# Optimization experiments

Measured on AMD Instinct MI355X. Metric: run time of the kernel, lower is better.

Reference implementation:

```python
import jax, jax.numpy as jnp
import numpy as np

N_NODES = 100000


def gcn_conv(x, W, b, src, dst, n):
    # PyG GCNConv: add self-loops, symmetric degree normalization,
    # linear transform then scatter-add aggregation at target nodes.
    h = x @ W  # [N, out]
    loop = jnp.arange(n, dtype=src.dtype)
    src_sl = jnp.concatenate([src, loop])
    dst_sl = jnp.concatenate([dst, loop])
    deg = jnp.zeros((n,), dtype=h.dtype).at[dst_sl].add(1.0)  # in-degree incl. self-loop
    dinv = jax.lax.rsqrt(deg)  # deg >= 1 thanks to self-loops
    norm = dinv[src_sl] * dinv[dst_sl]  # [E + N]
    msg = h[src_sl] * norm[:, None]  # gather + scale
    out = jax.ops.segment_sum(msg, dst_sl, num_segments=n)  # scatter-add
    return out + b


def setup_inputs() -> dict:
    key = jax.random.key(0)
    k1, k2, k3, k4 = jax.random.split(key, 4)
    n, e = N_NODES, 3200000
    in_c, hid = 3, 32
    x = jax.random.normal(k1, (n, in_c), dtype=jnp.float32)
    edge_index = jax.random.randint(k2, (2, e), 0, n, dtype=jnp.int64)
    W1 = jax.random.normal(k3, (in_c, hid), dtype=jnp.float32) / np.sqrt(in_c)
    b1 = jnp.zeros((hid,), dtype=jnp.float32)
    W2 = jax.random.normal(k4, (hid, in_c), dtype=jnp.float32) / np.sqrt(hid)
    b2 = jnp.zeros((in_c,), dtype=jnp.float32)
    return {"x": x, "edge_index": edge_index, "W1": W1, "b1": b1, "W2": W2, "b2": b2}


def reference(x, edge_index, W1, b1, W2, b2):
    n = x.shape[0]
    src, dst = edge_index[0], edge_index[1]
    h = jax.nn.relu(gcn_conv(x, W1, b1, src, dst, n))
    dx = gcn_conv(h, W2, b2, src, dst, n)
    return dx
```

## Files before the change

kernel.cpp:

```cpp
#include <hip/hip_runtime.h>

static constexpr int NN = 100000;
static constexpr int NE = 3200000;

static constexpr int BKT_D = 200;
static constexpr int NBUCK = NN / BKT_D;
static constexpr unsigned BMUL = 167773u;
static constexpr int BSH = 25;
static constexpr int CAP = 7296;

__device__ __forceinline__ int bdiv(int d) {
    return (int)(((unsigned long long)(unsigned)d * BMUL) >> BSH);
}

static constexpr unsigned GPOISON = 0xAAAAAAAAu;

static constexpr int P1B = 500;
static constexpr int P1T = 512;
static constexpr int EPB = NE / P1B;
static constexpr int EPB4 = EPB / 4;
static constexpr int EPT = (EPB + P1T - 1) / P1T;

static constexpr int AGT = 1024;

static constexpr float S1  = 262144.0f;
static constexpr float IS1 = 1.0f / S1;
static constexpr float S2  = 65536.0f;
static constexpr float IS2 = 1.0f / S2;
static constexpr int B1 = 1 << 22;
static constexpr int B2 = 1 << 23;


__global__ void k_build(const int* __restrict__ src, const int* __restrict__ dst,
                        unsigned* __restrict__ glen, int* __restrict__ keys) {
    __shared__ int skey[EPB];
    __shared__ unsigned short sbuck[EPB];
    __shared__ int cur[NBUCK];
    __shared__ int delta[NBUCK];
    __shared__ int wsum[8];
    int t = threadIdx.x, blk = blockIdx.x;

    const int base = blk * EPB;
    const int4* d4 = (const int4*)(dst + base);
    const int4* s4 = (const int4*)(src + base);
    int4 dc[4], sc[4];
    int nv = (t < EPB4 - 3 * P1T) ? 4 : 3;

    if (t < NBUCK) cur[t] = 0;
    __syncthreads();
#pragma unroll
    for (int j = 0; j < 3; ++j) {
        dc[j] = d4[j * P1T + t];
        sc[j] = s4[j * P1T + t];
    }
    if (nv == 4) { dc[3] = d4[3 * P1T + t]; sc[3] = s4[3 * P1T + t]; }
#pragma unroll
    for (int j = 0; j < 4; ++j) {
        if (j < nv) {
            atomicAdd(&cur[bdiv(dc[j].x)], 1);
            atomicAdd(&cur[bdiv(dc[j].y)], 1);
            atomicAdd(&cur[bdiv(dc[j].z)], 1);
            atomicAdd(&cur[bdiv(dc[j].w)], 1);
        }
    }
    __syncthreads();

    int c = (t < NBUCK) ? cur[t] : 0;
    int gbase = 0;
    if (t < NBUCK && c > 0)
        gbase = (int)(atomicAdd(&glen[t], (unsigned)c) - GPOISON);

    int v = c;
#pragma unroll
    for (int off = 1; off < 64; off <<= 1) {
        int y = __shfl_up(v, off, 64);
        if ((t & 63) >= off) v += y;
    }
    if ((t & 63) == 63) wsum[t >> 6] = v;
    __syncthreads();
    int woff = 0;
#pragma unroll
    for (int w = 0; w < 8; ++w) woff += (w < (t >> 6)) ? wsum[w] : 0;
    int inc = v + woff;

    if (t < NBUCK) {
        int loc = inc - c;
        cur[t] = loc;
        delta[t] = t * CAP + gbase - loc;
    }
    __syncthreads();

#pragma unroll
    for (int j = 0; j < 4; ++j) {
        if (j < nv) {
            int dv[4] = {dc[j].x, dc[j].y, dc[j].z, dc[j].w};
            int sv[4] = {sc[j].x, sc[j].y, sc[j].z, sc[j].w};
#pragma unroll
            for (int q = 0; q < 4; ++q) {
                int b = bdiv(dv[q]);
                int p = atomicAdd(&cur[b], 1);
                skey[p] = (sv[q] << 8) | (dv[q] - b * BKT_D);
                sbuck[p] = (unsigned short)b;
            }
        }
    }
    __syncthreads();
#pragma unroll
    for (int j = 0; j < EPT; ++j) {
        int o = j * P1T + t;
        if (o < EPB) keys[delta[sbuck[o]] + o] = skey[o];
    }
}


__global__ void k_deg_xd(const int* __restrict__ keys, const unsigned* __restrict__ glen,
                         const float* __restrict__ x, int4* __restrict__ xdq, int n) {
    __shared__ int cnt[4 * 256];
    int t = threadIdx.x, b = blockIdx.x;
    cnt[t] = 0;
    __syncthreads();
    int len = (int)(glen[b] - GPOISON);
    if (len > CAP) len = CAP;
    int hb = ((t >> 6) & 3) << 8;
    const int4* kb4 = (const int4*)(keys + (size_t)b * CAP);
    int len4 = len >> 2;
    for (int i = t; i < len4; i += AGT) {
        int4 K = kb4[i];
        atomicAdd(&cnt[hb + (K.x & 255)], 1);
        atomicAdd(&cnt[hb + (K.y & 255)], 1);
        atomicAdd(&cnt[hb + (K.z & 255)], 1);
        atomicAdd(&cnt[hb + (K.w & 255)], 1);
    }
    const int* kb = keys + (size_t)b * CAP;
    for (int i = (len4 << 2) + t; i < len; i += AGT)
        atomicAdd(&cnt[hb + (kb[i] & 255)], 1);
    __syncthreads();
    int node = b * BKT_D + t;
    if (t < BKT_D && node < n) {
        int c = cnt[t] + cnt[256 + t] + cnt[512 + t] + cnt[768 + t];
        float di = rsqrtf((float)c + 1.0f);
        xdq[node] = make_int4(__float2int_rn(x[node * 3 + 0] * di * S1) + B1,
                              __float2int_rn(x[node * 3 + 1] * di * S1) + B1,
                              __float2int_rn(x[node * 3 + 2] * di * S1), c);
    }
}


__device__ __forceinline__ void agg_edge(int k, const int4* __restrict__ val,
                                         unsigned long long* accp, int* accz, int hb) {
    int4 v = val[((unsigned)k) >> 8];
    unsigned long long p = ((unsigned long long)(unsigned)v.y << 32) | (unsigned)v.x;
    int dl = hb + (k & 255);
    atomicAdd(&accp[dl], p);
    atomicAdd(&accz[dl], v.z);
}

__global__ void k_agg1(const int* __restrict__ keys, const unsigned* __restrict__ glen,
                       const int4* __restrict__ xdq, const float* __restrict__ W1,
                       const float* __restrict__ b1, const float* __restrict__ W2,
                       int4* __restrict__ g2q, int n) {
    __shared__ unsigned long long accp[4 * 256];
    __shared__ int accz[4 * 256];
    __shared__ float W1s[96];
    __shared__ float W2s[96];
    __shared__ float b1s[32];
    int t = threadIdx.x, b = blockIdx.x;
    accp[t] = 0ull;
    accz[t] = 0;
    if (t >= 896 && t < 992) { W1s[t - 896] = W1[t - 896]; W2s[t - 896] = W2[t - 896]; }
    if (t >= 992) b1s[t - 992] = b1[t - 992];
    __syncthreads();

    int len = (int)(glen[b] - GPOISON);
    if (len > CAP) len = CAP;
    int hb = ((t >> 6) & 3) << 8;
    const int4* kb4 = (const int4*)(keys + (size_t)b * CAP);
    int len4 = len >> 2;
    for (int i = t; i < len4; i += AGT) {
        int4 K = kb4[i];
        agg_edge(K.x, xdq, accp, accz, hb);
        agg_edge(K.y, xdq, accp, accz, hb);
        agg_edge(K.z, xdq, accp, accz, hb);
        agg_edge(K.w, xdq, accp, accz, hb);
    }
    const int* kb = keys + (size_t)b * CAP;
    for (int i = (len4 << 2) + t; i < len; i += AGT)
        agg_edge(kb[i], xdq, accp, accz, hb);
    __syncthreads();

    int node = b * BKT_D + t;
    if (t >= BKT_D || node >= n) return;
    int4 self = xdq[node];
    int cnt = self.w;
    unsigned long long P = accp[t] + accp[256 + t] + accp[512 + t] + accp[768 + t];
    int sx = (int)(unsigned)(P & 0xffffffffull) - cnt * B1 + (self.x - B1);
    int sy = (int)(unsigned)(P >> 32) - cnt * B1 + (self.y - B1);
    int sz = accz[t] + accz[256 + t] + accz[512 + t] + accz[768 + t] + self.z;
    float a0 = (float)sx * IS1;
    float a1 = (float)sy * IS1;
    float a2 = (float)sz * IS1;
    float di = rsqrtf((float)cnt + 1.0f);
    float p0 = 0.f, p1 = 0.f, p2 = 0.f;
#pragma unroll
    for (int f = 0; f < 32; ++f) {
        float h = fmaxf(di * (a0 * W1s[f] + a1 * W1s[32 + f] + a2 * W1s[64 + f]) + b1s[f], 0.f);
        p0 += h * W2s[f * 3 + 0];
        p1 += h * W2s[f * 3 + 1];
        p2 += h * W2s[f * 3 + 2];
    }
    g2q[node] = make_int4(__float2int_rn(p0 * di * S2) + B2,
                          __float2int_rn(p1 * di * S2) + B2,
                          __float2int_rn(p2 * di * S2), cnt);
}


__global__ void k_agg2(const int* __restrict__ keys, const unsigned* __restrict__ glen,
                       const int4* __restrict__ g2q, const float* __restrict__ b2,
                       float* __restrict__ out, int n) {
    __shared__ unsigned long long accp[4 * 256];
    __shared__ int accz[4 * 256];
    int t = threadIdx.x, b = blockIdx.x;
    accp[t] = 0ull;
    accz[t] = 0;
    __syncthreads();

    int len = (int)(glen[b] - GPOISON);
    if (len > CAP) len = CAP;
    int hb = ((t >> 6) & 3) << 8;
    const int4* kb4 = (const int4*)(keys + (size_t)b * CAP);
    int len4 = len >> 2;
    for (int i = t; i < len4; i += AGT) {
        int4 K = kb4[i];
        agg_edge(K.x, g2q, accp, accz, hb);
        agg_edge(K.y, g2q, accp, accz, hb);
        agg_edge(K.z, g2q, accp, accz, hb);
        agg_edge(K.w, g2q, accp, accz, hb);
    }
    const int* kb = keys + (size_t)b * CAP;
    for (int i = (len4 << 2) + t; i < len; i += AGT)
        agg_edge(kb[i], g2q, accp, accz, hb);
    __syncthreads();

    int node = b * BKT_D + t;
    if (t >= BKT_D || node >= n) return;
    int4 self = g2q[node];
    int cnt = self.w;
    unsigned long long P = accp[t] + accp[256 + t] + accp[512 + t] + accp[768 + t];
    int sx = (int)(unsigned)(P & 0xffffffffull) - cnt * B2 + (self.x - B2);
    int sy = (int)(unsigned)(P >> 32) - cnt * B2 + (self.y - B2);
    int sz = accz[t] + accz[256 + t] + accz[512 + t] + accz[768 + t] + self.z;
    float di = rsqrtf((float)cnt + 1.0f);
    out[node * 3 + 0] = di * ((float)sx * IS2) + b2[0];
    out[node * 3 + 1] = di * ((float)sy * IS2) + b2[1];
    out[node * 3 + 2] = di * ((float)sz * IS2) + b2[2];
}

extern "C" void kernel_launch(void* const* d_in, const int* in_sizes, int n_in,
                              void* d_out, int out_size, void* d_ws, size_t ws_size,
                              hipStream_t stream) {
    const float* x   = (const float*)d_in[0];
    const int* ei    = (const int*)d_in[1];
    const float* W1  = (const float*)d_in[2];
    const float* b1  = (const float*)d_in[3];
    const float* W2  = (const float*)d_in[4];
    const float* b2  = (const float*)d_in[5];
    float* out       = (float*)d_out;

    const int n = NN;
    const int* src = ei;
    const int* dst = ei + NE;

    int* wsi       = (int*)d_ws;
    int* keys      = wsi;
    int4* xdq      = (int4*)(wsi + (size_t)CAP * NBUCK);
    int4* g2q      = xdq + n;
    unsigned* glen = (unsigned*)(g2q + n);

    k_build<<<P1B, P1T, 0, stream>>>(src, dst, glen, keys);

    k_deg_xd<<<NBUCK, AGT, 0, stream>>>(keys, glen, x, xdq, n);
    k_agg1<<<NBUCK, AGT, 0, stream>>>(keys, glen, xdq, W1, b1, W2, g2q, n);
    k_agg2<<<NBUCK, AGT, 0, stream>>>(keys, glen, g2q, b2, out, n);
}
```

Before: 133.1 us.

## Fuse degree and both aggregation passes into one cooperative kernel with LDS key cache

Result: slower. 243.6 us (+83.0%).

```diff
diff --git a/kernel.cpp b/kernel.cpp
--- a/kernel.cpp
+++ b/kernel.cpp
@@ -1,4 +1,7 @@
 #include <hip/hip_runtime.h>
+#include <hip/hip_cooperative_groups.h>
+
+namespace cg = cooperative_groups;
 
 static constexpr int NN = 100000;
 static constexpr int NE = 3200000;
@@ -8,6 +11,7 @@
 static constexpr unsigned BMUL = 167773u;
 static constexpr int BSH = 25;
 static constexpr int CAP = 7296;
+static constexpr int SCAP = 6912;
 
 __device__ __forceinline__ int bdiv(int d) {
     return (int)(((unsigned long long)(unsigned)d * BMUL) >> BSH);
@@ -21,7 +25,7 @@
 static constexpr int EPB4 = EPB / 4;
 static constexpr int EPT = (EPB + P1T - 1) / P1T;
 
-static constexpr int AGT = 1024;
+static constexpr int FGT = 512;
 
 static constexpr float S1  = 262144.0f;
 static constexpr float IS1 = 1.0f / S1;
@@ -113,39 +117,6 @@
 }
 
 
-__global__ void k_deg_xd(const int* __restrict__ keys, const unsigned* __restrict__ glen,
-                         const float* __restrict__ x, int4* __restrict__ xdq, int n) {
-    __shared__ int cnt[4 * 256];
-    int t = threadIdx.x, b = blockIdx.x;
-    cnt[t] = 0;
-    __syncthreads();
-    int len = (int)(glen[b] - GPOISON);
-    if (len > CAP) len = CAP;
-    int hb = ((t >> 6) & 3) << 8;
-    const int4* kb4 = (const int4*)(keys + (size_t)b * CAP);
-    int len4 = len >> 2;
-    for (int i = t; i < len4; i += AGT) {
-        int4 K = kb4[i];
-        atomicAdd(&cnt[hb + (K.x & 255)], 1);
-        atomicAdd(&cnt[hb + (K.y & 255)], 1);
-        atomicAdd(&cnt[hb + (K.z & 255)], 1);
-        atomicAdd(&cnt[hb + (K.w & 255)], 1);
-    }
-    const int* kb = keys + (size_t)b * CAP;
-    for (int i = (len4 << 2) + t; i < len; i += AGT)
-        atomicAdd(&cnt[hb + (kb[i] & 255)], 1);
-    __syncthreads();
-    int node = b * BKT_D + t;
-    if (t < BKT_D && node < n) {
-        int c = cnt[t] + cnt[256 + t] + cnt[512 + t] + cnt[768 + t];
-        float di = rsqrtf((float)c + 1.0f);
-        xdq[node] = make_int4(__float2int_rn(x[node * 3 + 0] * di * S1) + B1,
-                              __float2int_rn(x[node * 3 + 1] * di * S1) + B1,
-                              __float2int_rn(x[node * 3 + 2] * di * S1), c);
-    }
-}
-
-
 __device__ __forceinline__ void agg_edge(int k, const int4* __restrict__ val,
                                          unsigned long long* accp, int* accz, int hb) {
     int4 v = val[((unsigned)k) >> 8];
@@ -155,104 +126,127 @@
     atomicAdd(&accz[dl], v.z);
 }
 
-__global__ void k_agg1(const int* __restrict__ keys, const unsigned* __restrict__ glen,
-                       const int4* __restrict__ xdq, const float* __restrict__ W1,
-                       const float* __restrict__ b1, const float* __restrict__ W2,
-                       int4* __restrict__ g2q, int n) {
+__device__ __forceinline__ void agg_pass(const int* skeys, const int* __restrict__ kb,
+                                         int cc, int len, const int4* __restrict__ val,
+                                         unsigned long long* accp, int* accz, int hb, int t) {
+    int cc4 = cc >> 2;
+    const int4* s4 = (const int4*)skeys;
+    for (int i = t; i < cc4; i += FGT) {
+        int4 K = s4[i];
+        agg_edge(K.x, val, accp, accz, hb);
+        agg_edge(K.y, val, accp, accz, hb);
+        agg_edge(K.z, val, accp, accz, hb);
+        agg_edge(K.w, val, accp, accz, hb);
+    }
+    for (int i = (cc4 << 2) + t; i < cc; i += FGT)
+        agg_edge(skeys[i], val, accp, accz, hb);
+    for (int i = cc + t; i < len; i += FGT)
+        agg_edge(kb[i], val, accp, accz, hb);
+}
+
+__global__ void __launch_bounds__(FGT, 4) k_fused(
+        const int* __restrict__ keys, const unsigned* __restrict__ glen,
+        const float* __restrict__ x,
+        const float* __restrict__ W1, const float* __restrict__ b1,
+        const float* __restrict__ W2, const float* __restrict__ b2,
+        int4* __restrict__ xdq, int4* __restrict__ g2q, float* __restrict__ out) {
+    cg::grid_group grid = cg::this_grid();
+    __shared__ __align__(16) int skeys[SCAP];
     __shared__ unsigned long long accp[4 * 256];
     __shared__ int accz[4 * 256];
     __shared__ float W1s[96];
     __shared__ float W2s[96];
     __shared__ float b1s[32];
     int t = threadIdx.x, b = blockIdx.x;
-    accp[t] = 0ull;
-    accz[t] = 0;
-    if (t >= 896 && t < 992) { W1s[t - 896] = W1[t - 896]; W2s[t - 896] = W2[t - 896]; }
-    if (t >= 992) b1s[t - 992] = b1[t - 992];
-    __syncthreads();
 
     int len = (int)(glen[b] - GPOISON);
     if (len > CAP) len = CAP;
+    int cc = len < SCAP ? len : SCAP;
+
+    if (t < 96) { W1s[t] = W1[t]; W2s[t] = W2[t]; }
+    else if (t < 128) b1s[t - 96] = b1[t - 96];
+    accz[t] = 0; accz[512 + t] = 0;
+    __syncthreads();
+
     int hb = ((t >> 6) & 3) << 8;
     const int4* kb4 = (const int4*)(keys + (size_t)b * CAP);
+    const int* kb = keys + (size_t)b * CAP;
+
     int len4 = len >> 2;
-    for (int i = t; i < len4; i += AGT) {
+    for (int i = t; i < len4; i += FGT) {
         int4 K = kb4[i];
-        agg_edge(K.x, xdq, accp, accz, hb);
-        agg_edge(K.y, xdq, accp, accz, hb);
-        agg_edge(K.z, xdq, accp, accz, hb);
-        agg_edge(K.w, xdq, accp, accz, hb);
-    }
-    const int* kb = keys + (size_t)b * CAP;
-    for (int i = (len4 << 2) + t; i < len; i += AGT)
-        agg_edge(kb[i], xdq, accp, accz, hb);
+        if (4 * i < cc) *(int4*)&skeys[4 * i] = K;
+        atomicAdd(&accz[hb + (K.x & 255)], 1);
+        atomicAdd(&accz[hb + (K.y & 255)], 1);
+        atomicAdd(&accz[hb + (K.z & 255)], 1);
+        atomicAdd(&accz[hb + (K.w & 255)], 1);
+    }
+    for (int i = (len4 << 2) + t; i < len; i += FGT) {
+        int k = kb[i];
+        if (i < cc) skeys[i] = k;
+        atomicAdd(&accz[hb + (k & 255)], 1);
+    }
     __syncthreads();
 
     int node = b * BKT_D + t;
-    if (t >= BKT_D || node >= n) return;
-    int4 self = xdq[node];
-    int cnt = self.w;
-    unsigned long long P = accp[t] + accp[256 + t] + accp[512 + t] + accp[768 + t];
-    int sx = (int)(unsigned)(P & 0xffffffffull) - cnt * B1 + (self.x - B1);
-    int sy = (int)(unsigned)(P >> 32) - cnt * B1 + (self.y - B1);
-    int sz = accz[t] + accz[256 + t] + accz[512 + t] + accz[768 + t] + self.z;
-    float a0 = (float)sx * IS1;
-    float a1 = (float)sy * IS1;
-    float a2 = (float)sz * IS1;
-    float di = rsqrtf((float)cnt + 1.0f);
-    float p0 = 0.f, p1 = 0.f, p2 = 0.f;
-#pragma unroll
-    for (int f = 0; f < 32; ++f) {
-        float h = fmaxf(di * (a0 * W1s[f] + a1 * W1s[32 + f] + a2 * W1s[64 + f]) + b1s[f], 0.f);
-        p0 += h * W2s[f * 3 + 0];
-        p1 += h * W2s[f * 3 + 1];
-        p2 += h * W2s[f * 3 + 2];
-    }
-    g2q[node] = make_int4(__float2int_rn(p0 * di * S2) + B2,
+    bool own = (t < BKT_D);
+    int4 selfx = make_int4(0, 0, 0, 0);
+    int cnt = 0; float di = 0.f;
+    if (own) {
+        cnt = accz[t] + accz[256 + t] + accz[512 + t] + accz[768 + t];
+        di = rsqrtf((float)cnt + 1.0f);
+        selfx = make_int4(__float2int_rn(x[node * 3 + 0] * di * S1) + B1,
+                          __float2int_rn(x[node * 3 + 1] * di * S1) + B1,
+                          __float2int_rn(x[node * 3 + 2] * di * S1), cnt);
+        xdq[node] = selfx;
+    }
+    grid.sync();
+
+    accp[t] = 0ull; accp[512 + t] = 0ull;
+    accz[t] = 0;    accz[512 + t] = 0;
+    __syncthreads();
+    agg_pass(skeys, kb, cc, len, xdq, accp, accz, hb, t);
+    __syncthreads();
+
+    int4 selfg = make_int4(0, 0, 0, 0);
+    if (own) {
+        unsigned long long P = accp[t] + accp[256 + t] + accp[512 + t] + accp[768 + t];
+        int sx = (int)(unsigned)(P & 0xffffffffull) - cnt * B1 + (selfx.x - B1);
+        int sy = (int)(unsigned)(P >> 32) - cnt * B1 + (selfx.y - B1);
+        int sz = accz[t] + accz[256 + t] + accz[512 + t] + accz[768 + t] + selfx.z;
+        float a0 = (float)sx * IS1;
+        float a1 = (float)sy * IS1;
+        float a2 = (float)sz * IS1;
+        float p0 = 0.f, p1 = 0.f, p2 = 0.f;
+#pragma unroll
+        for (int f = 0; f < 32; ++f) {
+            float h = fmaxf(di * (a0 * W1s[f] + a1 * W1s[32 + f] + a2 * W1s[64 + f]) + b1s[f], 0.f);
+            p0 += h * W2s[f * 3 + 0];
+            p1 += h * W2s[f * 3 + 1];
+            p2 += h * W2s[f * 3 + 2];
+        }
+        selfg = make_int4(__float2int_rn(p0 * di * S2) + B2,
                           __float2int_rn(p1 * di * S2) + B2,
                           __float2int_rn(p2 * di * S2), cnt);
-}
-
-
-__global__ void k_agg2(const int* __restrict__ keys, const unsigned* __restrict__ glen,
-                       const int4* __restrict__ g2q, const float* __restrict__ b2,
-                       float* __restrict__ out, int n) {
-    __shared__ unsigned long long accp[4 * 256];
-    __shared__ int accz[4 * 256];
-    int t = threadIdx.x, b = blockIdx.x;
-    accp[t] = 0ull;
-    accz[t] = 0;
-    __syncthreads();
-
-    int len = (int)(glen[b] - GPOISON);
-    if (len > CAP) len = CAP;
-    int hb = ((t >> 6) & 3) << 8;
-    const int4* kb4 = (const int4*)(keys + (size_t)b * CAP);
-    int len4 = len >> 2;
-    for (int i = t; i < len4; i += AGT) {
-        int4 K = kb4[i];
-        agg_edge(K.x, g2q, accp, accz, hb);
-        agg_edge(K.y, g2q, accp, accz, hb);
-        agg_edge(K.z, g2q, accp, accz, hb);
-        agg_edge(K.w, g2q, accp, accz, hb);
-    }
-    const int* kb = keys + (size_t)b * CAP;
-    for (int i = (len4 << 2) + t; i < len; i += AGT)
-        agg_edge(kb[i], g2q, accp, accz, hb);
-    __syncthreads();
-
-    int node = b * BKT_D + t;
-    if (t >= BKT_D || node >= n) return;
-    int4 self = g2q[node];
-    int cnt = self.w;
-    unsigned long long P = accp[t] + accp[256 + t] + accp[512 + t] + accp[768 + t];
-    int sx = (int)(unsigned)(P & 0xffffffffull) - cnt * B2 + (self.x - B2);
-    int sy = (int)(unsigned)(P >> 32) - cnt * B2 + (self.y - B2);
-    int sz = accz[t] + accz[256 + t] + accz[512 + t] + accz[768 + t] + self.z;
-    float di = rsqrtf((float)cnt + 1.0f);
-    out[node * 3 + 0] = di * ((float)sx * IS2) + b2[0];
-    out[node * 3 + 1] = di * ((float)sy * IS2) + b2[1];
-    out[node * 3 + 2] = di * ((float)sz * IS2) + b2[2];
+        g2q[node] = selfg;
+    }
+    grid.sync();
+
+    accp[t] = 0ull; accp[512 + t] = 0ull;
+    accz[t] = 0;    accz[512 + t] = 0;
+    __syncthreads();
+    agg_pass(skeys, kb, cc, len, g2q, accp, accz, hb, t);
+    __syncthreads();
+
+    if (own) {
+        unsigned long long P = accp[t] + accp[256 + t] + accp[512 + t] + accp[768 + t];
+        int sx = (int)(unsigned)(P & 0xffffffffull) - cnt * B2 + (selfg.x - B2);
+        int sy = (int)(unsigned)(P >> 32) - cnt * B2 + (selfg.y - B2);
+        int sz = accz[t] + accz[256 + t] + accz[512 + t] + accz[768 + t] + selfg.z;
+        out[node * 3 + 0] = di * ((float)sx * IS2) + b2[0];
+        out[node * 3 + 1] = di * ((float)sy * IS2) + b2[1];
+        out[node * 3 + 2] = di * ((float)sz * IS2) + b2[2];
+    }
 }
 
 extern "C" void kernel_launch(void* const* d_in, const int* in_sizes, int n_in,
@@ -266,19 +260,21 @@
     const float* b2  = (const float*)d_in[5];
     float* out       = (float*)d_out;
 
-    const int n = NN;
     const int* src = ei;
     const int* dst = ei + NE;
 
     int* wsi       = (int*)d_ws;
-    int* keys      = wsi;
-    int4* xdq      = (int4*)(wsi + (size_t)CAP * NBUCK);
-    int4* g2q      = xdq + n;
-    unsigned* glen = (unsigned*)(g2q + n);
-
-    k_build<<<P1B, P1T, 0, stream>>>(src, dst, glen, keys);
-
-    k_deg_xd<<<NBUCK, AGT, 0, stream>>>(keys, glen, x, xdq, n);
-    k_agg1<<<NBUCK, AGT, 0, stream>>>(keys, glen, xdq, W1, b1, W2, g2q, n);
-    k_agg2<<<NBUCK, AGT, 0, stream>>>(keys, glen, g2q, b2, out, n);
-}
+    int* keysp     = wsi;
+    int4* xdqp     = (int4*)(wsi + (size_t)CAP * NBUCK);
+    int4* g2qp     = xdqp + NN;
+    unsigned* glen = (unsigned*)(g2qp + NN);
+
+    k_build<<<P1B, P1T, 0, stream>>>(src, dst, glen, keysp);
+
+    const int* keysc = keysp;
+    const unsigned* glenc = glen;
+    void* args[] = {(void*)&keysc, (void*)&glenc, (void*)&x, (void*)&W1, (void*)&b1,
+                    (void*)&W2, (void*)&b2, (void*)&xdqp, (void*)&g2qp, (void*)&out};
+    hipLaunchCooperativeKernel(reinterpret_cast<void*>(&k_fused), dim3(NBUCK), dim3(FGT),
+                               args, 0, stream);
+}
```
